# Kernel optimization log

Measured on AMD Instinct MI355X. Metric: run time of the kernel, lower is better.

The kernel has to match this reference:

```python
import jax, jax.numpy as jnp
import numpy as np

B, T, C = 1, 2048, 2048
H, KH, HD = 16, 4, 128  # n_head, n_kv_head, head_dim
ROPE_BASE = 10000.0


def setup_inputs() -> dict:
    key = jax.random.key(0)
    ks = jax.random.split(key, 5)
    s = 0.02
    return {
        "x": jax.random.normal(ks[0], (B, T, C), jnp.float32),
        "Wq": jax.random.normal(ks[1], (C, H * HD), jnp.float32) * s,
        "Wk": jax.random.normal(ks[2], (C, KH * HD), jnp.float32) * s,
        "Wv": jax.random.normal(ks[3], (C, KH * HD), jnp.float32) * s,
        "Wo": jax.random.normal(ks[4], (H * HD, C), jnp.float32) * s,
        "position_ids": jnp.arange(T, dtype=jnp.int32),
    }


def _rotate_half(a):
    h = a.shape[-1] // 2
    return jnp.concatenate([-a[..., h:], a[..., :h]], axis=-1)


def reference(x, Wq, Wk, Wv, Wo, position_ids):
    b, t, c = x.shape
    n_rep = H // KH
    # projections -> [B, heads, T, HD]
    q = (x @ Wq).reshape(b, t, H, HD).transpose(0, 2, 1, 3)
    k = (x @ Wk).reshape(b, t, KH, HD).transpose(0, 2, 1, 3)
    v = (x @ Wv).reshape(b, t, KH, HD).transpose(0, 2, 1, 3)
    # rotary embedding cache [T, HD]
    inv_freq = 1.0 / (ROPE_BASE ** (jnp.arange(0, HD, 2, dtype=jnp.float32) / HD))
    pos = jnp.arange(t, dtype=jnp.float32)
    freqs = pos[:, None] * inv_freq[None, :]
    emb = jnp.concatenate([freqs, freqs], axis=-1)
    cos = jnp.cos(emb)[position_ids][None, None]  # [1,1,T,HD]
    sin = jnp.sin(emb)[position_ids][None, None]
    q = q * cos + _rotate_half(q) * sin
    k = k * cos + _rotate_half(k) * sin
    # GQA: group query heads instead of materializing repeated K/V
    qg = q.reshape(b, KH, n_rep, t, HD)
    scale = jnp.float32(1.0 / np.sqrt(HD))
    scores = jnp.einsum('bgrtd,bgsd->bgrts', qg, k) * scale
    causal = jnp.tril(jnp.ones((t, t), dtype=bool))
    scores = jnp.where(causal, scores, jnp.float32(-1e30))
    p = jax.nn.softmax(scores, axis=-1)
    y = jnp.einsum('bgrts,bgsd->bgrtd', p, v)
    y = y.reshape(b, H, t, HD).transpose(0, 2, 1, 3).reshape(b, t, H * HD)
    return y @ Wo
```

## Files before the change

### kernel.cpp

```cpp
#include <hip/hip_runtime.h>

typedef unsigned short u16;
using bf16x8 = __attribute__((ext_vector_type(8))) short;
using f32x4  = __attribute__((ext_vector_type(4))) float;

#define GLD16(g, l)                                                            \
  __builtin_amdgcn_global_load_lds(                                            \
      (const __attribute__((address_space(1))) void*)(g),                      \
      (__attribute__((address_space(3))) void*)(l), 16, 0, 0)

__device__ __forceinline__ u16 f2b(float x) {
  union { float f; unsigned u; } v; v.f = x;
  unsigned r = v.u + 0x7FFF + ((v.u >> 16) & 1);
  return (u16)(r >> 16);
}

__global__ void cast_bf16_kernel(const float* __restrict__ in,
                                 u16* __restrict__ out, int n4) {
  int i = blockIdx.x * blockDim.x + threadIdx.x;
  int stride = gridDim.x * blockDim.x;
  for (; i < n4; i += stride) {
    float4 v = ((const float4*)in)[i];
    ushort4 o;
    o.x = f2b(v.x); o.y = f2b(v.y); o.z = f2b(v.z); o.w = f2b(v.w);
    ((ushort4*)out)[i] = o;
  }
}

__global__ void transpose_w_kernel(const float* __restrict__ src,
                                   u16* __restrict__ dst, int K, int N) {
  __shared__ float tile[32][33];
  int n0 = blockIdx.x * 32, k0 = blockIdx.y * 32;
  int tx = threadIdx.x, ty = threadIdx.y;
#pragma unroll
  for (int r = 0; r < 4; r++)
    tile[ty + r * 8][tx] = src[(size_t)(k0 + ty + r * 8) * N + n0 + tx];
  __syncthreads();
#pragma unroll
  for (int r = 0; r < 4; r++)
    dst[(size_t)(n0 + ty + r * 8) * K + k0 + tx] = f2b(tile[tx][ty + r * 8]);
}

__global__ void transpose_v_kernel(const u16* __restrict__ src,
                                   u16* __restrict__ dst) {
  __shared__ u16 tile[32][33];
  int h = blockIdx.z;
  int t0 = blockIdx.x * 32, d0 = blockIdx.y * 32;
  const u16* s = src + (size_t)h * 2048 * 128;
  u16* d = dst + (size_t)h * 128 * 2048;
  int tx = threadIdx.x, ty = threadIdx.y;
#pragma unroll
  for (int r = 0; r < 4; r++)
    tile[ty + r * 8][tx] = s[(size_t)(t0 + ty + r * 8) * 128 + d0 + tx];
  __syncthreads();
#pragma unroll
  for (int r = 0; r < 4; r++)
    d[(size_t)(d0 + ty + r * 8) * 2048 + t0 + tx] = tile[tx][ty + r * 8];
}

__global__ __launch_bounds__(256, 2)
void gemm_bt_128(const u16* __restrict__ A, const u16* __restrict__ Bt,
                 float* __restrict__ C, int M, int N, int K) {
  __shared__ u16 As[4][128 * 32];
  __shared__ u16 Bs[4][128 * 32];
  const int tid = threadIdx.x;
  const int lane = tid & 63;
  const int w = tid >> 6;
  const int wr = w >> 1, wc = w & 1;
  const int m0 = blockIdx.y * 128, n0 = blockIdx.x * 128;

  f32x4 acc[4][4] = {};

  const int srow = tid >> 2, skg = tid & 3;
  const u16* Ag0 = A + (size_t)(m0 + srow) * K + skg * 8;
  const u16* Ag1 = A + (size_t)(m0 + 64 + srow) * K + skg * 8;
  const u16* Bg0 = Bt + (size_t)(n0 + srow) * K + skg * 8;
  const u16* Bg1 = Bt + (size_t)(n0 + 64 + srow) * K + skg * 8;

  const int l0 = tid * 8, l1 = (256 + tid) * 8;
  u16 *pa0 = As[0], *pa1 = As[1], *pa2 = As[2], *pa3 = As[3];
  u16 *pb0 = Bs[0], *pb1 = Bs[1], *pb2 = Bs[2], *pb3 = Bs[3];

#define GSTAGE(k0v, pa, pb)                                                    \
  {                                                                            \
    GLD16(Ag0 + (k0v), (pa) + l0);                                             \
    GLD16(Ag1 + (k0v), (pa) + l1);                                             \
    GLD16(Bg0 + (k0v), (pb) + l0);                                             \
    GLD16(Bg1 + (k0v), (pb) + l1);                                             \
  }

  GSTAGE(0, pa0, pb0);
  GSTAGE(32, pa1, pb1);

  const int frow = lane & 15, fk = (lane >> 4) * 8;
  const int nk = K >> 5;

  for (int i = 0; i < nk; ++i) {
    if (i + 2 < nk) {
      GSTAGE((i + 2) * 32, pa2, pb2);
      asm volatile("s_waitcnt vmcnt(8)" ::: "memory");
    } else if (i + 1 < nk) {
      asm volatile("s_waitcnt vmcnt(4)" ::: "memory");
    } else {
      asm volatile("s_waitcnt vmcnt(0)" ::: "memory");
    }
    __builtin_amdgcn_s_barrier();
    __builtin_amdgcn_sched_barrier(0);
    bf16x8 av[4], bv[4];
#pragma unroll
    for (int m = 0; m < 4; m++)
      av[m] = *(const bf16x8*)(pa0 + (wr * 64 + m * 16 + frow) * 32 + fk);
#pragma unroll
    for (int n = 0; n < 4; n++)
      bv[n] = *(const bf16x8*)(pb0 + (wc * 64 + n * 16 + frow) * 32 + fk);
#pragma unroll
    for (int m = 0; m < 4; m++)
#pragma unroll
      for (int n = 0; n < 4; n++)
        acc[m][n] =
            __builtin_amdgcn_mfma_f32_16x16x32_bf16(av[m], bv[n], acc[m][n], 0, 0, 0);
    u16* t;
    t = pa0; pa0 = pa1; pa1 = pa2; pa2 = pa3; pa3 = t;
    t = pb0; pb0 = pb1; pb1 = pb2; pb2 = pb3; pb3 = t;
  }
#undef GSTAGE

  const int crow = (lane >> 4) * 4, ccol = lane & 15;
#pragma unroll
  for (int m = 0; m < 4; m++)
#pragma unroll
    for (int n = 0; n < 4; n++)
#pragma unroll
      for (int r = 0; r < 4; r++)
        C[(size_t)(m0 + wr * 64 + m * 16 + crow + r) * N +
          (n0 + wc * 64 + n * 16 + ccol)] = acc[m][n][r];
}

__global__ void rope_kernel(const float* __restrict__ QKV,
                            const int* __restrict__ pos, u16* __restrict__ Qb,
                            u16* __restrict__ Kb, u16* __restrict__ Vb) {
  const int t = blockIdx.x, tid = threadIdx.x;
  const float p = (float)pos[t];
  const float* row = QKV + (size_t)t * 3072;
  const float qscale = 0.08838834764831845f;
  const float c0 = -0.015625f * 13.287712379549449f;
#pragma unroll
  for (int i = 0; i < 4; i++) {
    int idx = tid + i * 256;
    int head = idx >> 6, d = idx & 63;
    float inv = exp2f((float)d * c0);
    float ang = p * inv;
    float s = sinf(ang), c = cosf(ang);
    float a0 = row[head * 128 + d], a1 = row[head * 128 + d + 64];
    Qb[((size_t)head * 2048 + t) * 128 + d] = f2b((a0 * c - a1 * s) * qscale);
    Qb[((size_t)head * 2048 + t) * 128 + d + 64] = f2b((a1 * c + a0 * s) * qscale);
  }
  {
    int head = tid >> 6, d = tid & 63;
    float inv = exp2f((float)d * c0);
    float ang = p * inv;
    float s = sinf(ang), c = cosf(ang);
    float a0 = row[2048 + head * 128 + d], a1 = row[2048 + head * 128 + d + 64];
    Kb[((size_t)head * 2048 + t) * 128 + d] = f2b(a0 * c - a1 * s);
    Kb[((size_t)head * 2048 + t) * 128 + d + 64] = f2b(a1 * c + a0 * s);
  }
#pragma unroll
  for (int i = 0; i < 2; i++) {
    int e = tid + i * 256;
    int kh = e >> 7, d = e & 127;
    Vb[((size_t)kh * 2048 + t) * 128 + d] = f2b(row[2560 + e]);
  }
}

__global__ __launch_bounds__(256, 2)
void attn_kernel(const u16* __restrict__ Qb, const u16* __restrict__ Kb,
                 const u16* __restrict__ Vtb, u16* __restrict__ Y) {
  __shared__ u16 Ks[2][64 * 128];
  __shared__ u16 Vs[2][128 * 64];
  __shared__ u16 Ps[4][16 * 64];
  const int tid = threadIdx.x, lane = tid & 63, w = tid >> 6;
  const int h = blockIdx.y, g = h >> 2;
  const int frow = lane & 15, fgrp = lane >> 4;
  const int t0 = blockIdx.x;
  const int t1 = 31 - t0;
  const int n0p = t0 + 1;

  const u16* Kg = Kb + (size_t)g * 2048 * 128;
  const u16* Vg = Vtb + (size_t)g * 128 * 2048;

#define STAGE(j0v, B)                                                          \
  {                                                                            \
    _Pragma("unroll")                                                          \
    for (int i = 0; i < 4; i++) {                                              \
      int p = tid + i * 256;                                                   \
      int kr = p >> 4, kc = (p & 15) ^ (kr & 7);                               \
      GLD16(Kg + (size_t)((j0v) + kr) * 128 + kc * 8, &Ks[B][p * 8]);          \
      int vr = p >> 3, vc = (p & 7) ^ (vr & 7);                                \
      GLD16(Vg + (size_t)vr * 2048 + (j0v) + vc * 8, &Vs[B][p * 8]);           \
    }                                                                          \
  }

  int qw = t0 * 64 + w * 16;
  bf16x8 qf[4];
  {
    const u16* Qrow = Qb + ((size_t)h * 2048 + (qw + frow)) * 128 + fgrp * 8;
#pragma unroll
    for (int kf = 0; kf < 4; kf++) qf[kf] = *(const bf16x8*)(Qrow + kf * 32);
  }

  f32x4 o[8] = {};
  float mrow[4], lrow[4];
#pragma unroll
  for (int r = 0; r < 4; r++) { mrow[r] = -1e30f; lrow[r] = 0.f; }

  STAGE(0, 0);
  __syncthreads();

  for (int it = 0; it < 33; ++it) {
    const int buf = it & 1;
    if (it + 1 < 33) {
      const int itn = it + 1;
      const int jn = (itn < n0p) ? itn : itn - n0p;
      STAGE(jn * 64, buf ^ 1);
    }
    if (it == n0p) {
#pragma unroll
      for (int r = 0; r < 4; r++) {
        float inv = 1.0f / lrow[r];
        int t = qw + fgrp * 4 + r;
#pragma unroll
        for (int db = 0; db < 8; db++)
          Y[(size_t)t * 2048 + h * 128 + db * 16 + frow] = f2b(o[db][r] * inv);
      }
#pragma unroll
      for (int db = 0; db < 8; db++)
#pragma unroll
        for (int r = 0; r < 4; r++) o[db][r] = 0.f;
#pragma unroll
      for (int r = 0; r < 4; r++) { mrow[r] = -1e30f; lrow[r] = 0.f; }
      qw = t1 * 64 + w * 16;
      const u16* Qrow = Qb + ((size_t)h * 2048 + (qw + frow)) * 128 + fgrp * 8;
#pragma unroll
      for (int kf = 0; kf < 4; kf++) qf[kf] = *(const bf16x8*)(Qrow + kf * 32);
    }
    const bool diag = (it == t0) || (it == 32);

    f32x4 sc[4] = {};
#pragma unroll
    for (int c = 0; c < 4; c++)
#pragma unroll
      for (int kf = 0; kf < 4; kf++) {
        int row = c * 16 + frow;
        bf16x8 kv = *(const bf16x8*)(
            &Ks[buf][row * 128 + ((kf * 4 + fgrp) ^ (row & 7)) * 8]);
        sc[c] = __builtin_amdgcn_mfma_f32_16x16x32_bf16(qf[kf], kv, sc[c], 0, 0, 0);
      }
    if (diag) {
#pragma unroll
      for (int c = 0; c < 4; c++) {
        int j = c * 16 + frow;
#pragma unroll
        for (int r = 0; r < 4; r++)
          if (j > (w * 16 + fgrp * 4 + r)) sc[c][r] = -1e30f;
      }
    }
    float pm[4];
#pragma unroll
    for (int r = 0; r < 4; r++)
      pm[r] = fmaxf(fmaxf(sc[0][r], sc[1][r]), fmaxf(sc[2][r], sc[3][r]));
#pragma unroll
    for (int off = 1; off < 16; off <<= 1)
#pragma unroll
      for (int r = 0; r < 4; r++) pm[r] = fmaxf(pm[r], __shfl_xor(pm[r], off, 64));
    bool nd = false;
#pragma unroll
    for (int r = 0; r < 4; r++) nd = nd || (pm[r] > mrow[r] + 8.f);
    if (__any(nd)) {
#pragma unroll
      for (int r = 0; r < 4; r++) {
        float mn = fmaxf(mrow[r], pm[r]);
        float alpha = __expf(mrow[r] - mn);
        mrow[r] = mn;
        lrow[r] *= alpha;
#pragma unroll
        for (int db = 0; db < 8; db++) o[db][r] *= alpha;
      }
    }
    float rs[4];
#pragma unroll
    for (int r = 0; r < 4; r++) {
      float s = 0.f;
#pragma unroll
      for (int c = 0; c < 4; c++) { sc[c][r] = __expf(sc[c][r] - mrow[r]); s += sc[c][r]; }
      rs[r] = s;
    }
#pragma unroll
    for (int off = 1; off < 16; off <<= 1)
#pragma unroll
      for (int r = 0; r < 4; r++) rs[r] += __shfl_xor(rs[r], off, 64);
#pragma unroll
    for (int r = 0; r < 4; r++) lrow[r] += rs[r];
    u16* Pw = Ps[w];
#pragma unroll
    for (int c = 0; c < 4; c++)
#pragma unroll
      for (int r = 0; r < 4; r++) {
        int row = fgrp * 4 + r, col = c * 16 + frow;
        Pw[row * 64 + (((col >> 3) ^ row) & 7) * 8 + (col & 7)] = f2b(sc[c][r]);
      }
    asm volatile("s_waitcnt lgkmcnt(0)" ::: "memory");
    bf16x8 pf[2];
#pragma unroll
    for (int ks = 0; ks < 2; ks++)
      pf[ks] = *(const bf16x8*)(
          &Pw[frow * 64 + ((ks * 4 + fgrp) ^ (frow & 7)) * 8]);
#pragma unroll
    for (int db = 0; db < 8; db++)
#pragma unroll
      for (int ks = 0; ks < 2; ks++) {
        int row = db * 16 + frow;
        bf16x8 vf = *(const bf16x8*)(
            &Vs[buf][row * 64 + ((ks * 4 + fgrp) ^ (row & 7)) * 8]);
        o[db] = __builtin_amdgcn_mfma_f32_16x16x32_bf16(pf[ks], vf, o[db], 0, 0, 0);
      }
    __syncthreads();
  }
#pragma unroll
  for (int r = 0; r < 4; r++) {
    float inv = 1.0f / lrow[r];
    int t = qw + fgrp * 4 + r;
#pragma unroll
    for (int db = 0; db < 8; db++)
      Y[(size_t)t * 2048 + h * 128 + db * 16 + frow] = f2b(o[db][r] * inv);
  }
#undef STAGE
}

extern "C" void kernel_launch(void* const* d_in, const int* in_sizes, int n_in,
                              void* d_out, int out_size, void* d_ws,
                              size_t ws_size, hipStream_t stream) {
  const float* x  = (const float*)d_in[0];
  const float* Wq = (const float*)d_in[1];
  const float* Wk = (const float*)d_in[2];
  const float* Wv = (const float*)d_in[3];
  const float* Wo = (const float*)d_in[4];
  const int* pos  = (const int*)d_in[5];
  float* out = (float*)d_out;
  char* ws = (char*)d_ws;

  u16* xb      = (u16*)(ws + 0);
  u16* Wqkv_bt = (u16*)(ws + 8388608);
  u16* Wo_bt   = (u16*)(ws + 20971520);
  float* QKV   = (float*)(ws + 29360128);
  u16* Yb      = (u16*)(ws + 29360128);
  u16* Qb      = (u16*)(ws + 54525952);
  u16* Kb      = (u16*)(ws + 62914560);
  u16* Vb      = (u16*)(ws + 65011712);
  u16* Vtb     = (u16*)(ws + 67108864);

  cast_bf16_kernel<<<1024, 256, 0, stream>>>(x, xb, 2048 * 2048 / 4);
  transpose_w_kernel<<<dim3(64, 64), dim3(32, 8), 0, stream>>>(Wq, Wqkv_bt, 2048, 2048);
  transpose_w_kernel<<<dim3(16, 64), dim3(32, 8), 0, stream>>>(Wk, Wqkv_bt + (size_t)2048 * 2048, 2048, 512);
  transpose_w_kernel<<<dim3(16, 64), dim3(32, 8), 0, stream>>>(Wv, Wqkv_bt + (size_t)2560 * 2048, 2048, 512);
  transpose_w_kernel<<<dim3(64, 64), dim3(32, 8), 0, stream>>>(Wo, Wo_bt, 2048, 2048);

  gemm_bt_128<<<dim3(3072 / 128, 2048 / 128), 256, 0, stream>>>(xb, Wqkv_bt, QKV, 2048, 3072, 2048);

  rope_kernel<<<2048, 256, 0, stream>>>(QKV, pos, Qb, Kb, Vb);
  transpose_v_kernel<<<dim3(64, 4, 4), dim3(32, 8), 0, stream>>>(Vb, Vtb);

  attn_kernel<<<dim3(16, 16), 256, 0, stream>>>(Qb, Kb, Vtb, Yb);

  gemm_bt_128<<<dim3(2048 / 128, 2048 / 128), 256, 0, stream>>>(Yb, Wo_bt, out, 2048, 2048, 2048);
}
```

Measured before the change: 263.8 us.

## Split attention KV loop across two interleaved partitions and combine partial softmax results

Attention blocks now run in two z-slices, each handling every other KV tile (even or odd), doubling grid size from 256 to 512 blocks to improve occupancy on the many-CU GPU. Each slice writes a normalized bf16 partial output plus per-row max and sum, and a new combine kernel merges them with log-sum-exp weights. This adds an extra kernel launch, extra global traffic for partials, and an extra bf16 rounding step. It reuses the xb/weights workspace region for the partial outputs, which is safe because those buffers are dead by then.

```diff
diff --git a/kernel.cpp b/kernel.cpp
--- a/kernel.cpp
+++ b/kernel.cpp
@@ -13,6 +13,9 @@
   union { float f; unsigned u; } v; v.f = x;
   unsigned r = v.u + 0x7FFF + ((v.u >> 16) & 1);
   return (u16)(r >> 16);
+}
+__device__ __forceinline__ float b2f(u16 x) {
+  union { unsigned u; float f; } v; v.u = (unsigned)x << 16; return v.f;
 }
 
 __global__ void cast_bf16_kernel(const float* __restrict__ in,
@@ -174,16 +177,20 @@
 
 __global__ __launch_bounds__(256, 2)
 void attn_kernel(const u16* __restrict__ Qb, const u16* __restrict__ Kb,
-                 const u16* __restrict__ Vtb, u16* __restrict__ Y) {
+                 const u16* __restrict__ Vtb, u16* __restrict__ Op,
+                 float* __restrict__ ml) {
   __shared__ u16 Ks[2][64 * 128];
   __shared__ u16 Vs[2][128 * 64];
   __shared__ u16 Ps[4][16 * 64];
   const int tid = threadIdx.x, lane = tid & 63, w = tid >> 6;
   const int h = blockIdx.y, g = h >> 2;
+  const int z = blockIdx.z;
   const int frow = lane & 15, fgrp = lane >> 4;
   const int t0 = blockIdx.x;
   const int t1 = 31 - t0;
-  const int n0p = t0 + 1;
+  const int c0 = (t0 >= z) ? ((t0 - z) >> 1) + 1 : 0;
+  const int c1 = ((t1 - z) >> 1) + 1;
+  const int nit = c0 + c1;
 
   const u16* Kg = Kb + (size_t)g * 2048 * 128;
   const u16* Vg = Vtb + (size_t)g * 128 * 2048;
@@ -200,6 +207,23 @@
     }                                                                          \
   }
 
+#define FLUSH()                                                                \
+  {                                                                            \
+    _Pragma("unroll")                                                          \
+    for (int r = 0; r < 4; r++) {                                              \
+      float inv = lrow[r] > 0.f ? 1.0f / lrow[r] : 0.f;                        \
+      int t = qw + fgrp * 4 + r;                                               \
+      _Pragma("unroll")                                                        \
+      for (int db = 0; db < 8; db++)                                           \
+        Op[(size_t)z * 4194304 + (size_t)t * 2048 + h * 128 + db * 16 + frow] =\
+            f2b(o[db][r] * inv);                                               \
+      if (frow == 0) {                                                         \
+        int mi = (((z * 16 + h) * 2048) + t) * 2;                              \
+        ml[mi] = mrow[r]; ml[mi + 1] = lrow[r];                                \
+      }                                                                        \
+    }                                                                          \
+  }
+
   int qw = t0 * 64 + w * 16;
   bf16x8 qf[4];
   {
@@ -213,25 +237,18 @@
 #pragma unroll
   for (int r = 0; r < 4; r++) { mrow[r] = -1e30f; lrow[r] = 0.f; }
 
-  STAGE(0, 0);
+  STAGE(z * 64, 0);
   __syncthreads();
 
-  for (int it = 0; it < 33; ++it) {
+  for (int it = 0; it < nit; ++it) {
     const int buf = it & 1;
-    if (it + 1 < 33) {
+    if (it + 1 < nit) {
       const int itn = it + 1;
-      const int jn = (itn < n0p) ? itn : itn - n0p;
+      const int jn = (itn < c0) ? z + 2 * itn : z + 2 * (itn - c0);
       STAGE(jn * 64, buf ^ 1);
     }
-    if (it == n0p) {
-#pragma unroll
-      for (int r = 0; r < 4; r++) {
-        float inv = 1.0f / lrow[r];
-        int t = qw + fgrp * 4 + r;
-#pragma unroll
-        for (int db = 0; db < 8; db++)
-          Y[(size_t)t * 2048 + h * 128 + db * 16 + frow] = f2b(o[db][r] * inv);
-      }
+    if (it == c0) {
+      FLUSH();
 #pragma unroll
       for (int db = 0; db < 8; db++)
 #pragma unroll
@@ -243,7 +260,9 @@
 #pragma unroll
       for (int kf = 0; kf < 4; kf++) qf[kf] = *(const bf16x8*)(Qrow + kf * 32);
     }
-    const bool diag = (it == t0) || (it == 32);
+    const int pass = (it < c0) ? 0 : 1;
+    const int j = (pass == 0) ? z + 2 * it : z + 2 * (it - c0);
+    const bool diag = (pass == 0) ? (j == t0) : (j == t1);
 
     f32x4 sc[4] = {};
 #pragma unroll
@@ -258,10 +277,10 @@
     if (diag) {
 #pragma unroll
       for (int c = 0; c < 4; c++) {
-        int j = c * 16 + frow;
+        int jj = c * 16 + frow;
 #pragma unroll
         for (int r = 0; r < 4; r++)
-          if (j > (w * 16 + fgrp * 4 + r)) sc[c][r] = -1e30f;
+          if (jj > (w * 16 + fgrp * 4 + r)) sc[c][r] = -1e30f;
       }
     }
     float pm[4];
@@ -325,15 +344,35 @@
       }
     __syncthreads();
   }
-#pragma unroll
-  for (int r = 0; r < 4; r++) {
-    float inv = 1.0f / lrow[r];
-    int t = qw + fgrp * 4 + r;
-#pragma unroll
-    for (int db = 0; db < 8; db++)
-      Y[(size_t)t * 2048 + h * 128 + db * 16 + frow] = f2b(o[db][r] * inv);
-  }
+  FLUSH();
 #undef STAGE
+#undef FLUSH
+}
+
+__global__ void attn_combine_kernel(const u16* __restrict__ Op,
+                                    const float* __restrict__ ml,
+                                    u16* __restrict__ Y) {
+  int u = blockIdx.x * blockDim.x + threadIdx.x;
+  int t = u >> 4, h = u & 15;
+  int i0 = ((0 * 16 + h) * 2048 + t) * 2;
+  int i1 = ((1 * 16 + h) * 2048 + t) * 2;
+  float m0 = ml[i0], l0 = ml[i0 + 1];
+  float m1 = ml[i1], l1 = ml[i1 + 1];
+  float m = fmaxf(m0, m1);
+  float w0 = __expf(m0 - m) * l0, w1 = __expf(m1 - m) * l1;
+  float inv = 1.0f / (w0 + w1);
+  w0 *= inv; w1 *= inv;
+  size_t base = (size_t)t * 2048 + h * 128;
+#pragma unroll
+  for (int i = 0; i < 16; i++) {
+    bf16x8 a = *(const bf16x8*)(Op + base + i * 8);
+    bf16x8 b = *(const bf16x8*)(Op + 4194304 + base + i * 8);
+    bf16x8 out;
+#pragma unroll
+    for (int jj = 0; jj < 8; jj++)
+      out[jj] = (short)f2b(w0 * b2f((u16)a[jj]) + w1 * b2f((u16)b[jj]));
+    *(bf16x8*)(Y + base + i * 8) = out;
+  }
 }
 
 extern "C" void kernel_launch(void* const* d_in, const int* in_sizes, int n_in,
@@ -357,6 +396,8 @@
   u16* Kb      = (u16*)(ws + 62914560);
   u16* Vb      = (u16*)(ws + 65011712);
   u16* Vtb     = (u16*)(ws + 67108864);
+  u16* Op      = (u16*)(ws + 0);
+  float* ml    = (float*)(ws + 16777216);
 
   cast_bf16_kernel<<<1024, 256, 0, stream>>>(x, xb, 2048 * 2048 / 4);
   transpose_w_kernel<<<dim3(64, 64), dim3(32, 8), 0, stream>>>(Wq, Wqkv_bt, 2048, 2048);
@@ -369,7 +410,8 @@
   rope_kernel<<<2048, 256, 0, stream>>>(QKV, pos, Qb, Kb, Vb);
   transpose_v_kernel<<<dim3(64, 4, 4), dim3(32, 8), 0, stream>>>(Vb, Vtb);
 
-  attn_kernel<<<dim3(16, 16), 256, 0, stream>>>(Qb, Kb, Vtb, Yb);
+  attn_kernel<<<dim3(16, 16, 2), 256, 0, stream>>>(Qb, Kb, Vtb, Op, ml);
+  attn_combine_kernel<<<128, 256, 0, stream>>>(Op, ml, Yb);
 
   gemm_bt_128<<<dim3(2048 / 128, 2048 / 128), 256, 0, stream>>>(Yb, Wo_bt, out, 2048, 2048, 2048);
 }
```

Result: faster. 255.4 us (-3.2%).
